# Kernel tuning notes

Measured on AMD Instinct MI355X. Metric: run time of the kernel, lower is better.

Reference implementation:

```python
import jax, jax.numpy as jnp
import numpy as np

N_POST = 50000   # dense_shape[0], number of postsynaptic neurons
N_IN = 17400     # dense_shape[1], number of input (LGN) units
NNZ = 1000000    # number of synapses
N_SYN_BASIS = 5  # receptor basis functions
N_SYN_TYPES = 10


def setup_inputs() -> dict:
    key = jax.random.key(0)
    k1, k2, k3, k4, k5, k6 = jax.random.split(key, 6)
    inp = jax.random.normal(k1, (1, 64, N_IN), dtype=jnp.float32)
    rows = jax.random.randint(k2, (NNZ,), 0, N_POST)
    cols = jax.random.randint(k3, (NNZ,), 0, N_IN)
    indices = jnp.stack([rows, cols], axis=1).astype(jnp.int64)  # [nnz, 2]
    input_weights = jax.random.normal(k4, (NNZ,), dtype=jnp.float32)
    synaptic_weights = jax.random.uniform(k5, (N_SYN_TYPES, N_SYN_BASIS), dtype=jnp.float32)
    syn_ids = jax.random.randint(k6, (NNZ,), 0, N_SYN_TYPES).astype(jnp.int64)
    return {"inp": inp, "indices": indices, "input_weights": input_weights,
            "synaptic_weights": synaptic_weights, "syn_ids": syn_ids}


def reference(inp, indices, input_weights, synaptic_weights, syn_ids):
    B, T, n_in = inp.shape
    tokens = B * T
    x = inp.reshape(tokens, n_in)              # flatten (batch, time)
    rows = indices[:, 0]
    cols = indices[:, 1]
    # per-synapse receptor factors: synaptic_weights[syn_ids] -> [nnz, n_basis]
    factors = jnp.take(synaptic_weights, syn_ids, axis=0)
    # gather presynaptic activity once for all receptor bases: [nnz, tokens]
    g = jnp.take(x.T, cols, axis=0)
    outs = []
    for r in range(N_SYN_BASIS):
        vals = input_weights * factors[:, r]                      # [nnz]
        contrib = g * vals[:, None]                               # [nnz, tokens]
        # sparse-dense matmul == segment-sum over destination rows
        out_r = jax.ops.segment_sum(contrib, rows, num_segments=N_POST)  # [n_post, tokens]
        outs.append(out_r)
    i_in = jnp.stack(outs, axis=0)                                # [n_basis, n_post, tokens]
    # tf.transpose of 3D reverses dims -> [tokens, n_post, n_basis]
    out = jnp.transpose(i_in, (2, 1, 0)).reshape(B, T, N_POST * N_SYN_BASIS)
    return out
```

## Files before the change

kernel.cpp:

```cpp
#include <hip/hip_runtime.h>
#include <hip/hip_fp16.h>

#define N_POST 50000
#define N_IN   17400
#define NNZ_E  1000000
#define T_DIM  64
#define R_DIM  5
#define NT_DIM 10

#define BROWS  256
#define NBUCK  ((N_POST + BROWS - 1) / BROWS)
#define EPB    4096
#define NBLK1  ((NNZ_E + EPB - 1) / EPB)
#define CAP    64
#define FCAP   5632
#define CAPR   7168
#define CTILES ((N_IN + 63) / 64)
#define RECBUF_N 1024

static __device__ __forceinline__ unsigned pack2h(float a, float b) {
    __half2 h = __floats2half2_rn(a, b);
    return *reinterpret_cast<unsigned*>(&h);
}

__global__ __launch_bounds__(256) void k_ts(const float* __restrict__ x,
                                            __half* __restrict__ xT,
                                            const int2* __restrict__ idx2,
                                            const float* __restrict__ iw,
                                            const int* __restrict__ sid,
                                            unsigned short* __restrict__ cnt,
                                            uint2* __restrict__ rec1) {
    __shared__ float tile[64][65];
    int bb = blockIdx.x;
    int tid = threadIdx.x;
    if (bb < CTILES) {
        int c0 = bb * 64;
        int l = tid & 63, w = tid >> 6;
        #pragma unroll
        for (int i = 0; i < 16; ++i) {
            int t = i * 4 + w;
            int c = c0 + l;
            tile[l][t] = (c < N_IN) ? x[t * N_IN + c] : 0.f;
        }
        __syncthreads();
        #pragma unroll
        for (int i = 0; i < 16; ++i) {
            int cc = i * 4 + w;
            int c = c0 + cc;
            if (c < N_IN) xT[c * 64 + l] = __float2half(tile[cc][l]);
        }
        return;
    }
    int* lcur = (int*)&tile[0][0];
    for (int i = tid; i < NBUCK; i += 256) lcur[i] = 0;
    __syncthreads();
    int blk = bb - CTILES;
    int base = blk * EPB;
    int n = min(EPB, NNZ_E - base);
    for (int i = tid; i < n; i += 256) {
        int2 rc = idx2[base + i];
        unsigned bk = (unsigned)rc.x >> 8;
        int pos = atomicAdd(&lcur[bk], 1);
        unsigned xx = (unsigned)rc.y | ((unsigned)sid[base + i] << 15)
                    | ((unsigned)(rc.x & 255) << 19);
        rec1[(bk * NBLK1 + blk) * CAP + pos] =
            make_uint2(xx, __float_as_uint(iw[base + i]));
    }
    __syncthreads();
    for (int i = tid; i < NBUCK; i += 256)
        cnt[i * NBLK1 + blk] = (unsigned short)lcur[i];
}

__global__ __launch_bounds__(512) void k_fine(const uint2* __restrict__ rec1,
                                              const unsigned short* __restrict__ cnt,
                                              const float* __restrict__ S,
                                              uint4* __restrict__ rec,
                                              int* __restrict__ rstart,
                                              int* __restrict__ plen) {
    __shared__ uint2 lrec[FCAP];
    __shared__ int scnt[256];
    __shared__ int soff[256];
    __shared__ int lhist[BROWS];
    __shared__ int lsc[BROWS];
    __shared__ int lcur[BROWS];
    __shared__ float s_S[NT_DIM * R_DIM];
    int t = threadIdx.x;
    int b = blockIdx.x;
    int pbase = b * CAPR;
    if (t < NT_DIM * R_DIM) s_S[t] = S[t];
    int cv = 0;
    if (t < 256) {
        cv = (t < NBLK1) ? (int)cnt[b * NBLK1 + t] : 0;
        scnt[t] = cv;
        soff[t] = cv;
        lhist[t] = 0;
    }
    __syncthreads();
    for (int off = 1; off < 256; off <<= 1) {
        int u = 0;
        if (t < 256 && t >= off) u = soff[t - off];
        __syncthreads();
        if (t < 256) soff[t] += u;
        __syncthreads();
    }
    if (t < 256) soff[t] -= cv;
    __syncthreads();
    const uint2* srcb = rec1 + (size_t)b * NBLK1 * CAP;
    for (int slot = t; slot < NBLK1 * CAP; slot += 512) {
        int cell = slot >> 6;
        int j = slot & 63;
        if (j < scnt[cell]) lrec[soff[cell] + j] = srcb[slot];
    }
    int nrec = soff[255] + scnt[255];
    __syncthreads();
    for (int i = t; i < nrec; i += 512)
        atomicAdd(&lhist[(lrec[i].x >> 19) & 255], 1);
    __syncthreads();
    int v = 0, vp = 0;
    if (t < 256) { v = lhist[t]; vp = (v + 3) & ~3; lsc[t] = vp; }
    __syncthreads();
    for (int off = 1; off < 256; off <<= 1) {
        int u = 0;
        if (t < 256 && t >= off) u = lsc[t - off];
        __syncthreads();
        if (t < 256) lsc[t] += u;
        __syncthreads();
    }
    if (t < 256) {
        int exclp = lsc[t] - vp;
        int p = b * BROWS + t;
        if (p < N_POST) { rstart[p] = pbase + exclp; plen[p] = vp; }
        lcur[t] = exclp;
    }
    __syncthreads();
    for (int i = t; i < nrec; i += 512) {
        uint2 rc = lrec[i];
        int r = (rc.x >> 19) & 255;
        int pos = atomicAdd(&lcur[r], 1);
        unsigned col = rc.x & 0x7FFF;
        const float* f = &s_S[((rc.x >> 15) & 0xF) * R_DIM];
        float w = __uint_as_float(rc.y);
        uint4 r4;
        r4.x = col << 7;
        r4.y = pack2h(w * f[0], w * f[1]);
        r4.z = pack2h(w * f[2], w * f[3]);
        r4.w = pack2h(w * f[4], 0.f);
        rec[pbase + pos] = r4;
    }
    if (t < 256) {
        int exclp = lsc[t] - vp;
        for (int u = v; u < vp; ++u)
            rec[pbase + exclp + u] = make_uint4(0, 0, 0, 0);
    }
}

#define FMAREC(Rk, Xk)                                                              \
    do {                                                                            \
        unsigned x_ = (Xk);                                                         \
        unsigned w01_ = (Rk).y, w23_ = (Rk).z, w4_ = (Rk).w;                        \
        asm("v_fma_mix_f32 %0, %1, %2, %0 op_sel:[0,0,0] op_sel_hi:[1,1,0]"         \
            : "+v"(a0e) : "v"(x_), "v"(w01_));                                      \
        asm("v_fma_mix_f32 %0, %1, %2, %0 op_sel:[1,0,0] op_sel_hi:[1,1,0]"         \
            : "+v"(a0o) : "v"(x_), "v"(w01_));                                      \
        asm("v_fma_mix_f32 %0, %1, %2, %0 op_sel:[0,1,0] op_sel_hi:[1,1,0]"         \
            : "+v"(a1e) : "v"(x_), "v"(w01_));                                      \
        asm("v_fma_mix_f32 %0, %1, %2, %0 op_sel:[1,1,0] op_sel_hi:[1,1,0]"         \
            : "+v"(a1o) : "v"(x_), "v"(w01_));                                      \
        asm("v_fma_mix_f32 %0, %1, %2, %0 op_sel:[0,0,0] op_sel_hi:[1,1,0]"         \
            : "+v"(a2e) : "v"(x_), "v"(w23_));                                      \
        asm("v_fma_mix_f32 %0, %1, %2, %0 op_sel:[1,0,0] op_sel_hi:[1,1,0]"         \
            : "+v"(a2o) : "v"(x_), "v"(w23_));                                      \
        asm("v_fma_mix_f32 %0, %1, %2, %0 op_sel:[0,1,0] op_sel_hi:[1,1,0]"         \
            : "+v"(a3e) : "v"(x_), "v"(w23_));                                      \
        asm("v_fma_mix_f32 %0, %1, %2, %0 op_sel:[1,1,0] op_sel_hi:[1,1,0]"         \
            : "+v"(a3o) : "v"(x_), "v"(w23_));                                      \
        asm("v_fma_mix_f32 %0, %1, %2, %0 op_sel:[0,0,0] op_sel_hi:[1,1,0]"         \
            : "+v"(a4e) : "v"(x_), "v"(w4_));                                       \
        asm("v_fma_mix_f32 %0, %1, %2, %0 op_sel:[1,0,0] op_sel_hi:[1,1,0]"         \
            : "+v"(a4o) : "v"(x_), "v"(w4_));                                       \
    } while (0)

#define ROWBODY(RP)                                                                 \
    do {                                                                            \
        if (0 < ng) {                                                               \
            R0 = (RP)[0]; R1 = (RP)[1]; R2 = (RP)[2]; R3 = (RP)[3];                 \
            X0 = *(const unsigned*)(xb + (R0.x + lane4));                           \
            X1 = *(const unsigned*)(xb + (R1.x + lane4));                           \
            X2 = *(const unsigned*)(xb + (R2.x + lane4));                           \
            X3 = *(const unsigned*)(xb + (R3.x + lane4));                           \
        } else {                                                                    \
            R0 = R1 = R2 = R3 = make_uint4(0, 0, 0, 0);                             \
            X0 = X1 = X2 = X3 = 0;                                                  \
        }                                                                           \
        for (int g = 1; g < ngmax; ++g) {                                           \
            uint4 S0, S1, S2, S3;                                                   \
            unsigned Y0, Y1, Y2, Y3;                                                \
            if (g < ng) {                                                           \
                S0 = (RP)[(g << 2)];     S1 = (RP)[(g << 2) + 1];                   \
                S2 = (RP)[(g << 2) + 2]; S3 = (RP)[(g << 2) + 3];                   \
                Y0 = *(const unsigned*)(xb + (S0.x + lane4));                       \
                Y1 = *(const unsigned*)(xb + (S1.x + lane4));                       \
                Y2 = *(const unsigned*)(xb + (S2.x + lane4));                       \
                Y3 = *(const unsigned*)(xb + (S3.x + lane4));                       \
            } else {                                                                \
                S0 = S1 = S2 = S3 = make_uint4(0, 0, 0, 0);                         \
                Y0 = Y1 = Y2 = Y3 = 0;                                              \
            }                                                                       \
            FMAREC(R0, X0); FMAREC(R1, X1); FMAREC(R2, X2); FMAREC(R3, X3);         \
            R0 = S0; R1 = S1; R2 = S2; R3 = S3;                                     \
            X0 = Y0; X1 = Y1; X2 = Y2; X3 = Y3;                                     \
        }                                                                           \
        if (ngmax > 0) {                                                            \
            FMAREC(R0, X0); FMAREC(R1, X1); FMAREC(R2, X2); FMAREC(R3, X3);         \
        }                                                                           \
    } while (0)

__global__ __launch_bounds__(256, 4) void k_phase2(
        const __half* __restrict__ xT, const int* __restrict__ rstart,
        const int* __restrict__ plen, const uint4* __restrict__ rec,
        float* __restrict__ out) {
    __shared__ float o_lds[T_DIM * 81];
    __shared__ uint4 recbuf[RECBUF_N];
    const char* xb = (const char*)xT;
    int tid = threadIdx.x;
    int wave = tid >> 6, lane = tid & 63;
    int half = lane >> 5;
    int lane4 = (lane & 31) * 4;
    int p0 = blockIdx.x * 16;
    int start0 = rstart[p0];
    int nblk = rstart[p0 + 15] + plen[p0 + 15] - start0;
    bool uselds = (nblk <= RECBUF_N);
    if (uselds) {
        for (int i = tid; i < nblk; i += 256) recbuf[i] = rec[start0 + i];
    }
    __syncthreads();
    #pragma unroll
    for (int h = 0; h < 2; ++h) {
        int pa = p0 + wave * 4 + h * 2;
        int myrow = pa + half;
        int ih = rstart[myrow];
        int ng = plen[myrow] >> 2;
        int na = plen[pa], nb = plen[pa + 1];
        int ngmax = __builtin_amdgcn_readfirstlane((na > nb ? na : nb) >> 2);
        float a0e = 0.f, a0o = 0.f, a1e = 0.f, a1o = 0.f, a2e = 0.f;
        float a2o = 0.f, a3e = 0.f, a3o = 0.f, a4e = 0.f, a4o = 0.f;
        uint4 R0, R1, R2, R3;
        unsigned X0, X1, X2, X3;
        if (uselds) {
            const uint4* rp = recbuf + (ih - start0);
            ROWBODY(rp);
        } else {
            const uint4* rp = rec + ih;
            ROWBODY(rp);
        }
        int rowl = wave * 4 + h * 2 + half;
        int t0 = (lane & 31) * 2;
        float* d0 = &o_lds[t0 * 81 + rowl * 5];
        d0[0] = a0e; d0[1] = a1e; d0[2] = a2e; d0[3] = a3e; d0[4] = a4e;
        float* d1 = &o_lds[(t0 + 1) * 81 + rowl * 5];
        d1[0] = a0o; d1[1] = a1o; d1[2] = a2o; d1[3] = a3o; d1[4] = a4o;
    }
    __syncthreads();
    int base5 = blockIdx.x * 80;
    for (int i2 = tid; i2 < T_DIM * 80; i2 += 256) {
        int t = i2 / 80;
        int j = i2 - t * 80;
        out[(size_t)t * (N_POST * R_DIM) + base5 + j] = o_lds[t * 81 + j];
    }
}

extern "C" void kernel_launch(void* const* d_in, const int* in_sizes, int n_in,
                              void* d_out, int out_size, void* d_ws, size_t ws_size,
                              hipStream_t stream) {
    const float* inp  = (const float*)d_in[0];
    const int2*  idx2 = (const int2*)d_in[1];
    const float* iw   = (const float*)d_in[2];
    const float* S    = (const float*)d_in[3];
    const int*   sid  = (const int*)d_in[4];
    float* out = (float*)d_out;

    char* ws = (char*)d_ws;
    size_t off = 0;
    auto alloc = [&](size_t bytes) -> void* {
        void* p = ws + off;
        off += (bytes + 255) & ~(size_t)255;
        return p;
    };
    __half* xT            = (__half*)alloc((size_t)N_IN * T_DIM * 2);
    unsigned short* cnt   = (unsigned short*)alloc((size_t)NBUCK * NBLK1 * 2);
    int*   rstart         = (int*)alloc((size_t)N_POST * 4);
    int*   plen           = (int*)alloc((size_t)N_POST * 4);
    uint2* rec1           = (uint2*)alloc((size_t)NBUCK * NBLK1 * CAP * 8);
    uint4* rec            = (uint4*)alloc((size_t)NBUCK * CAPR * 16);

    k_ts<<<CTILES + NBLK1, 256, 0, stream>>>(inp, xT, idx2, iw, sid, cnt, rec1);
    k_fine<<<NBUCK, 512, 0, stream>>>(rec1, cnt, S, rec, rstart, plen);
    k_phase2<<<N_POST / 16, 256, 0, stream>>>(xT, rstart, plen, rec, out);
}
```

Before: 74.68 us.

## Pad paired rows to equal length, double-buffer phase2 loads, widen k_ts blocks

In k_fine each row's padded length becomes the maximum of itself and its neighbour row (t^1). Both halves of a wave therefore process the same number of groups, and ng can be taken wave-uniform from one row. The phase2 inner loop is reworked into an A/B double-buffered scheme that unrolls two groups per iteration and drops the per-iteration zero-fill and conditional prefetch. k_ts is launched with 1024 threads per block instead of 256. The change adds padding records, which cost extra reads and FMAs on zero-weight entries in exchange for fewer divergence checks.

```diff
diff --git a/kernel.cpp b/kernel.cpp
--- a/kernel.cpp
+++ b/kernel.cpp
@@ -23,13 +23,13 @@
     return *reinterpret_cast<unsigned*>(&h);
 }
 
-__global__ __launch_bounds__(256) void k_ts(const float* __restrict__ x,
-                                            __half* __restrict__ xT,
-                                            const int2* __restrict__ idx2,
-                                            const float* __restrict__ iw,
-                                            const int* __restrict__ sid,
-                                            unsigned short* __restrict__ cnt,
-                                            uint2* __restrict__ rec1) {
+__global__ __launch_bounds__(1024) void k_ts(const float* __restrict__ x,
+                                             __half* __restrict__ xT,
+                                             const int2* __restrict__ idx2,
+                                             const float* __restrict__ iw,
+                                             const int* __restrict__ sid,
+                                             unsigned short* __restrict__ cnt,
+                                             uint2* __restrict__ rec1) {
     __shared__ float tile[64][65];
     int bb = blockIdx.x;
     int tid = threadIdx.x;
@@ -37,27 +37,27 @@
         int c0 = bb * 64;
         int l = tid & 63, w = tid >> 6;
         #pragma unroll
-        for (int i = 0; i < 16; ++i) {
-            int t = i * 4 + w;
+        for (int i = 0; i < 4; ++i) {
+            int t = i * 16 + w;
             int c = c0 + l;
             tile[l][t] = (c < N_IN) ? x[t * N_IN + c] : 0.f;
         }
         __syncthreads();
         #pragma unroll
-        for (int i = 0; i < 16; ++i) {
-            int cc = i * 4 + w;
+        for (int i = 0; i < 4; ++i) {
+            int cc = i * 16 + w;
             int c = c0 + cc;
             if (c < N_IN) xT[c * 64 + l] = __float2half(tile[cc][l]);
         }
         return;
     }
     int* lcur = (int*)&tile[0][0];
-    for (int i = tid; i < NBUCK; i += 256) lcur[i] = 0;
+    for (int i = tid; i < NBUCK; i += 1024) lcur[i] = 0;
     __syncthreads();
     int blk = bb - CTILES;
     int base = blk * EPB;
     int n = min(EPB, NNZ_E - base);
-    for (int i = tid; i < n; i += 256) {
+    for (int i = tid; i < n; i += 1024) {
         int2 rc = idx2[base + i];
         unsigned bk = (unsigned)rc.x >> 8;
         int pos = atomicAdd(&lcur[bk], 1);
@@ -67,7 +67,7 @@
             make_uint2(xx, __float_as_uint(iw[base + i]));
     }
     __syncthreads();
-    for (int i = tid; i < NBUCK; i += 256)
+    for (int i = tid; i < NBUCK; i += 1024)
         cnt[i * NBLK1 + blk] = (unsigned short)lcur[i];
 }
 
@@ -116,8 +116,14 @@
     for (int i = t; i < nrec; i += 512)
         atomicAdd(&lhist[(lrec[i].x >> 19) & 255], 1);
     __syncthreads();
+    if (t < 256) soff[t] = (lhist[t] + 3) & ~3;
+    __syncthreads();
     int v = 0, vp = 0;
-    if (t < 256) { v = lhist[t]; vp = (v + 3) & ~3; lsc[t] = vp; }
+    if (t < 256) {
+        v = lhist[t];
+        vp = max(soff[t], soff[t ^ 1]);
+        lsc[t] = vp;
+    }
     __syncthreads();
     for (int off = 1; off < 256; off <<= 1) {
         int u = 0;
@@ -180,38 +186,38 @@
             : "+v"(a4o) : "v"(x_), "v"(w4_));                                       \
     } while (0)
 
+#define LOADSET(P0, P1, P2, P3, XX0, XX1, XX2, XX3, q)                              \
+    do {                                                                            \
+        P0 = (q)[0]; P1 = (q)[1]; P2 = (q)[2]; P3 = (q)[3];                         \
+        XX0 = *(const unsigned*)(xb + (P0.x + lane4));                              \
+        XX1 = *(const unsigned*)(xb + (P1.x + lane4));                              \
+        XX2 = *(const unsigned*)(xb + (P2.x + lane4));                              \
+        XX3 = *(const unsigned*)(xb + (P3.x + lane4));                              \
+    } while (0)
+
 #define ROWBODY(RP)                                                                 \
     do {                                                                            \
-        if (0 < ng) {                                                               \
-            R0 = (RP)[0]; R1 = (RP)[1]; R2 = (RP)[2]; R3 = (RP)[3];                 \
-            X0 = *(const unsigned*)(xb + (R0.x + lane4));                           \
-            X1 = *(const unsigned*)(xb + (R1.x + lane4));                           \
-            X2 = *(const unsigned*)(xb + (R2.x + lane4));                           \
-            X3 = *(const unsigned*)(xb + (R3.x + lane4));                           \
-        } else {                                                                    \
-            R0 = R1 = R2 = R3 = make_uint4(0, 0, 0, 0);                             \
-            X0 = X1 = X2 = X3 = 0;                                                  \
-        }                                                                           \
-        for (int g = 1; g < ngmax; ++g) {                                           \
-            uint4 S0, S1, S2, S3;                                                   \
-            unsigned Y0, Y1, Y2, Y3;                                                \
+        if (ng > 0) {                                                               \
+            LOADSET(A0, A1, A2, A3, XA0, XA1, XA2, XA3, (RP));                      \
+            int g = 1;                                                              \
+            for (; g + 2 <= ng; g += 2) {                                           \
+                LOADSET(B0, B1, B2, B3, XB0, XB1, XB2, XB3, (RP) + (g << 2));       \
+                FMAREC(A0, XA0); FMAREC(A1, XA1);                                   \
+                FMAREC(A2, XA2); FMAREC(A3, XA3);                                   \
+                LOADSET(A0, A1, A2, A3, XA0, XA1, XA2, XA3, (RP) + ((g + 1) << 2)); \
+                FMAREC(B0, XB0); FMAREC(B1, XB1);                                   \
+                FMAREC(B2, XB2); FMAREC(B3, XB3);                                   \
+            }                                                                       \
             if (g < ng) {                                                           \
-                S0 = (RP)[(g << 2)];     S1 = (RP)[(g << 2) + 1];                   \
-                S2 = (RP)[(g << 2) + 2]; S3 = (RP)[(g << 2) + 3];                   \
-                Y0 = *(const unsigned*)(xb + (S0.x + lane4));                       \
-                Y1 = *(const unsigned*)(xb + (S1.x + lane4));                       \
-                Y2 = *(const unsigned*)(xb + (S2.x + lane4));                       \
-                Y3 = *(const unsigned*)(xb + (S3.x + lane4));                       \
+                LOADSET(B0, B1, B2, B3, XB0, XB1, XB2, XB3, (RP) + (g << 2));       \
+                FMAREC(A0, XA0); FMAREC(A1, XA1);                                   \
+                FMAREC(A2, XA2); FMAREC(A3, XA3);                                   \
+                FMAREC(B0, XB0); FMAREC(B1, XB1);                                   \
+                FMAREC(B2, XB2); FMAREC(B3, XB3);                                   \
             } else {                                                                \
-                S0 = S1 = S2 = S3 = make_uint4(0, 0, 0, 0);                         \
-                Y0 = Y1 = Y2 = Y3 = 0;                                              \
+                FMAREC(A0, XA0); FMAREC(A1, XA1);                                   \
+                FMAREC(A2, XA2); FMAREC(A3, XA3);                                   \
             }                                                                       \
-            FMAREC(R0, X0); FMAREC(R1, X1); FMAREC(R2, X2); FMAREC(R3, X3);         \
-            R0 = S0; R1 = S1; R2 = S2; R3 = S3;                                     \
-            X0 = Y0; X1 = Y1; X2 = Y2; X3 = Y3;                                     \
-        }                                                                           \
-        if (ngmax > 0) {                                                            \
-            FMAREC(R0, X0); FMAREC(R1, X1); FMAREC(R2, X2); FMAREC(R3, X3);         \
         }                                                                           \
     } while (0)
 
@@ -239,13 +245,11 @@
         int pa = p0 + wave * 4 + h * 2;
         int myrow = pa + half;
         int ih = rstart[myrow];
-        int ng = plen[myrow] >> 2;
-        int na = plen[pa], nb = plen[pa + 1];
-        int ngmax = __builtin_amdgcn_readfirstlane((na > nb ? na : nb) >> 2);
+        int ng = __builtin_amdgcn_readfirstlane(plen[pa]) >> 2;
         float a0e = 0.f, a0o = 0.f, a1e = 0.f, a1o = 0.f, a2e = 0.f;
         float a2o = 0.f, a3e = 0.f, a3o = 0.f, a4e = 0.f, a4o = 0.f;
-        uint4 R0, R1, R2, R3;
-        unsigned X0, X1, X2, X3;
+        uint4 A0, A1, A2, A3, B0, B1, B2, B3;
+        unsigned XA0, XA1, XA2, XA3, XB0, XB1, XB2, XB3;
         if (uselds) {
             const uint4* rp = recbuf + (ih - start0);
             ROWBODY(rp);
@@ -293,7 +297,7 @@
     uint2* rec1           = (uint2*)alloc((size_t)NBUCK * NBLK1 * CAP * 8);
     uint4* rec            = (uint4*)alloc((size_t)NBUCK * CAPR * 16);
 
-    k_ts<<<CTILES + NBLK1, 256, 0, stream>>>(inp, xT, idx2, iw, sid, cnt, rec1);
+    k_ts<<<CTILES + NBLK1, 1024, 0, stream>>>(inp, xT, idx2, iw, sid, cnt, rec1);
     k_fine<<<NBUCK, 512, 0, stream>>>(rec1, cnt, S, rec, rstart, plen);
     k_phase2<<<N_POST / 16, 256, 0, stream>>>(xT, rstart, plen, rec, out);
 }
```

Result: faster. 67.79 us (-9.2%).
